# Kernel tuning notes

Hardware: AMD Instinct MI355X
Metric: run time of the kernel (lower is better)

Reference implementation:

```python
import jax, jax.numpy as jnp
import numpy as np

N, K, D = 32768, 8192, 64


def setup_inputs() -> dict:
    key = jax.random.key(0)
    k1, k2, k3 = jax.random.split(key, 3)
    z = jax.random.normal(k1, (N, D), dtype=jnp.float32)
    # Riemannian sensitivity weight per sample (positive scalar from decoder VJP norms)
    g_weight = jax.random.uniform(k2, (N,), dtype=jnp.float32)
    # codebook: nn.Embedding(num_embeddings, embedding_dim), weight ~ N(0,1)
    embedding = jax.random.normal(k3, (K, D), dtype=jnp.float32)
    return {"z": z, "g_weight": g_weight, "embedding": embedding}


def reference(z, g_weight, embedding):
    # d(z, e) = ||z||^2 + ||e||^2 - 2 z e^T  -> [N, K]
    z_flat = z.reshape(-1, embedding.shape[1])
    distances = (
        jnp.sum(z_flat * z_flat, axis=1, keepdims=True)
        + jnp.sum(embedding * embedding, axis=1)
        - 2.0 * jnp.matmul(z_flat, embedding.T)
    )
    # Riemannian scaling: d_R = d * G(z)
    riemannian_distances = distances * g_weight[:, None]
    return jnp.argmin(riemannian_distances, axis=1)
```

## Files before the change

kernel.cpp:

```cpp
#include <hip/hip_runtime.h>
#include <hip/hip_fp16.h>
#include <cfloat>
#include <climits>


typedef short  s16x8  __attribute__((ext_vector_type(8)));
typedef float  f32x16 __attribute__((ext_vector_type(16)));

static constexpr int N_ = 32768;
static constexpr int K_ = 8192;
static constexpr int D_ = 64;
static constexpr int NTILES = K_ / 32;
static constexpr int REC_SLOTS = 576;
static constexpr size_t REC_BYTES = (size_t)NTILES * REC_SLOTS * 16;
static constexpr float FLAG_MARGIN = 0.001953125f;
static constexpr float RESID_SCALE = 1024.0f;
static constexpr float RESID_INV   = 0.0009765625f;

struct alignas(16) Part3 { float b1, b2; int i1, pad; };

__device__ __forceinline__ short f2h_s(float x) {
    __half h = __float2half(x);
    return (short)__half_as_short(h);
}
__device__ __forceinline__ float h2f_s(short s) {
    __half h = __short_as_half((unsigned short)s);
    return __half2float(h);
}

__global__ void rq_prep(const float* __restrict__ emb, s16x8* __restrict__ recs)
{
    __shared__ double sp[32][8];
    const int tile = blockIdx.x;
    const int t = threadIdx.x;
    const int c = t >> 3, q = t & 7;
    const int f = q >> 1, h = q & 1;
    const float* src = emb + (size_t)(tile * 32 + c) * D_ + q * 8;
    float4 a = ((const float4*)src)[0];
    float4 b = ((const float4*)src)[1];
    float e[8] = {a.x, a.y, a.z, a.w, b.x, b.y, b.z, b.w};
    s16x8 u1, u2;
    double s = 0.0;
    #pragma unroll
    for (int j = 0; j < 8; ++j) {
        __half h1 = __float2half(e[j]);
        float r = e[j] - __half2float(h1);
        u1[j] = (short)__half_as_short(h1);
        u2[j] = f2h_s(r * RESID_SCALE);
        s = fma((double)e[j], (double)e[j], s);
    }
    const size_t rb = (size_t)tile * REC_SLOTS;
    recs[rb + f * 64 + h * 32 + c] = u1;
    recs[rb + 320 + f * 64 + h * 32 + c] = u2;
    sp[c][q] = s;
    __syncthreads();
    if (t < 32) {
        double se = 0.0;
        #pragma unroll
        for (int j = 0; j < 8; ++j) se += sp[t][j];
        se *= 0.5;
        float sf = (float)se;
        __half sh = __float2half(sf);
        float  sr = sf - __half2float(sh);
        s16x8 v;
        #pragma unroll
        for (int j = 0; j < 8; ++j) v[j] = 0;
        v[0] = (short)__half_as_short(sh);
        v[1] = f2h_s(sr);
        recs[rb + 256 + t] = v;
    } else if (t < 64) {
        s16x8 v;
        #pragma unroll
        for (int j = 0; j < 8; ++j) v[j] = 0;
        recs[rb + 256 + t] = v;
    }
}

__global__ __launch_bounds__(256)
void rq_main(const float* __restrict__ z,
             const s16x8* __restrict__ recs,
             Part3* __restrict__ parts,
             int tpb )
{
    __shared__ s16x8 lbuf[2][REC_SLOTS];
    const int tid  = threadIdx.x;
    const int wave = tid >> 6, lane = tid & 63;
    const int col  = lane & 31, h = lane >> 5;
    const int slice = blockIdx.y;
    const int tile0 = slice * tpb;
    const int rowbase = blockIdx.x * 128 + wave * 32;
    const int zrow = rowbase + col;

    s16x8 zn1[4], zn2[4];
    #pragma unroll
    for (int f = 0; f < 4; ++f) {
        const float* src = z + (size_t)zrow * D_ + f * 16 + h * 8;
        float4 a = ((const float4*)src)[0];
        float4 b = ((const float4*)src)[1];
        float e[8] = {a.x, a.y, a.z, a.w, b.x, b.y, b.z, b.w};
        #pragma unroll
        for (int j = 0; j < 8; ++j) {
            float zn = -e[j];
            __half h1 = __float2half(zn);
            zn1[f][j] = (short)__half_as_short(h1);
            zn2[f][j] = f2h_s((zn - __half2float(h1)) * RESID_SCALE);
        }
    }
    s16x8 bse;
    #pragma unroll
    for (int j = 0; j < 8; ++j) bse[j] = 0;
    if (h == 0) { bse[0] = (short)0x3C00; bse[1] = (short)0x3C00; }

    {
        const size_t gb = (size_t)tile0 * REC_SLOTS;
        lbuf[0][tid]       = recs[gb + tid];
        lbuf[0][256 + tid] = recs[gb + 256 + tid];
        if (tid < 64) lbuf[0][512 + tid] = recs[gb + 512 + tid];
    }
    __syncthreads();

    float b1 = FLT_MAX, b2 = FLT_MAX;
    int   i1 = INT_MAX;

    for (int t = 0; t < tpb; ++t) {
        const int cb = t & 1, nb = cb ^ 1;
        const bool pf = (t + 1 < tpb);
        s16x8 r0, r1, r2;
        if (pf) {
            const size_t gb = (size_t)(tile0 + t + 1) * REC_SLOTS;
            r0 = recs[gb + tid];
            r1 = recs[gb + 256 + tid];
            if (tid < 64) r2 = recs[gb + 512 + tid];
        }

        s16x8 ea[4], e2a[4], sea;
        #pragma unroll
        for (int f = 0; f < 4; ++f) ea[f]  = lbuf[cb][f * 64 + lane];
        sea = lbuf[cb][256 + lane];
        #pragma unroll
        for (int f = 0; f < 4; ++f) e2a[f] = lbuf[cb][320 + f * 64 + lane];

        f32x16 acc, acc2;
        #pragma unroll
        for (int r = 0; r < 16; ++r) { acc[r] = 0.0f; acc2[r] = 0.0f; }
        #pragma unroll
        for (int f = 0; f < 4; ++f)
            acc = __builtin_amdgcn_mfma_f32_32x32x16_f16(ea[f], zn1[f], acc, 0, 0, 0);
        acc = __builtin_amdgcn_mfma_f32_32x32x16_f16(sea, bse, acc, 0, 0, 0);
        #pragma unroll
        for (int f = 0; f < 4; ++f)
            acc2 = __builtin_amdgcn_mfma_f32_32x32x16_f16(e2a[f], zn1[f], acc2, 0, 0, 0);
        #pragma unroll
        for (int f = 0; f < 4; ++f)
            acc2 = __builtin_amdgcn_mfma_f32_32x32x16_f16(ea[f], zn2[f], acc2, 0, 0, 0);

        const int cbase = (tile0 + t) * 32 + 4 * h;
        #pragma unroll
        for (int r = 0; r < 16; ++r) {
            float v = acc[r] + acc2[r] * RESID_INV;
            int cr = cbase + (r & 3) + 8 * (r >> 2);
            b2 = fminf(b2, fmaxf(v, b1));
            bool lt = v < b1;
            i1 = lt ? cr : i1;
            b1 = fminf(b1, v);
        }

        if (pf) {
            lbuf[nb][tid]       = r0;
            lbuf[nb][256 + tid] = r1;
            if (tid < 64) lbuf[nb][512 + tid] = r2;
        }
        __syncthreads();
    }

    float ob1 = __shfl_xor(b1, 32);
    float ob2 = __shfl_xor(b2, 32);
    int   oi1 = __shfl_xor(i1, 32);
    float nb2 = fminf(fminf(b2, ob2), fmaxf(b1, ob1));
    if (ob1 < b1 || (ob1 == b1 && oi1 < i1)) { b1 = ob1; i1 = oi1; }
    b2 = nb2;
    if (lane < 32) {
        Part3 p; p.b1 = b1; p.b2 = b2; p.i1 = i1; p.pad = 0;
        parts[(size_t)slice * N_ + (rowbase + lane)] = p;
    }
}

__global__ void rq_merge(const Part3* __restrict__ parts,
                         const float* __restrict__ g,
                         int* __restrict__ out,
                         int* __restrict__ counter,
                         int* __restrict__ list,
                         int nsl, int maxf)
{
    int row = blockIdx.x * 256 + threadIdx.x;
    Part3 p = parts[row];
    float b1 = p.b1, b2 = p.b2; int i1 = p.i1;
    for (int s = 1; s < nsl; ++s) {
        Part3 q = parts[(size_t)s * N_ + row];
        float m2 = fminf(fminf(b2, q.b2), fmaxf(b1, q.b1));
        if (q.b1 < b1) { b1 = q.b1; i1 = q.i1; }
        b2 = m2;
    }
    if (g[row] == 0.0f) { out[row] = 0; return; }
    out[row] = i1;
    if (b2 - b1 < FLAG_MARGIN) {
        int idx = atomicAdd(counter, 1);
        if (idx < maxf) list[idx] = row;
    }
}

__global__ __launch_bounds__(256)
void rq_cleanup_part(const float* __restrict__ z,
                     const float* __restrict__ emb,
                     const int* __restrict__ counter,
                     const int* __restrict__ list,
                     double* __restrict__ vparts,
                     int* __restrict__ iparts,
                     int maxf)
{
    int cnt = *counter; if (cnt > maxf) cnt = maxf;
    const int jobs = cnt * 8;
    const int wid  = (blockIdx.x * 256 + threadIdx.x) >> 6;
    const int lane = threadIdx.x & 63;
    const int nw   = gridDim.x * 4;

    for (int j = wid; j < jobs; j += nw) {
        const int row = list[j >> 3];
        const int sl  = j & 7;
        float zr[64];
        {
            const float4* zp = reinterpret_cast<const float4*>(z + (size_t)row * D_);
            #pragma unroll
            for (int q = 0; q < 16; ++q) {
                float4 v = zp[q];
                zr[4*q] = v.x; zr[4*q+1] = v.y; zr[4*q+2] = v.z; zr[4*q+3] = v.w;
            }
        }
        double bv = DBL_MAX; int bi = INT_MAX;
        for (int i = 0; i < 16; ++i) {
            const int c = sl * 1024 + i * 64 + lane;
            const float4* ep = reinterpret_cast<const float4*>(emb + (size_t)c * D_);
            double sd0 = 0, sd1 = 0, sq0 = 0, sq1 = 0;
            #pragma unroll
            for (int q = 0; q < 16; ++q) {
                float4 ev = ep[q];
                sd0 = fma((double)ev.x, (double)zr[4*q+0], sd0);
                sq0 = fma((double)ev.x, (double)ev.x, sq0);
                sd1 = fma((double)ev.y, (double)zr[4*q+1], sd1);
                sq1 = fma((double)ev.y, (double)ev.y, sq1);
                sd0 = fma((double)ev.z, (double)zr[4*q+2], sd0);
                sq0 = fma((double)ev.z, (double)ev.z, sq0);
                sd1 = fma((double)ev.w, (double)zr[4*q+3], sd1);
                sq1 = fma((double)ev.w, (double)ev.w, sq1);
            }
            double v = 0.5 * (sq0 + sq1) - (sd0 + sd1);
            if (v < bv) { bv = v; bi = c; }
        }
        #pragma unroll
        for (int m = 1; m < 64; m <<= 1) {
            double ov = __shfl_xor(bv, m);
            int    oi = __shfl_xor(bi, m);
            if (ov < bv || (ov == bv && oi < bi)) { bv = ov; bi = oi; }
        }
        if (lane == 0) { vparts[j] = bv; iparts[j] = bi; }
    }
}

__global__ void rq_cleanup_fin(const int* __restrict__ counter,
                               const int* __restrict__ list,
                               const double* __restrict__ vparts,
                               const int* __restrict__ iparts,
                               int* __restrict__ out, int maxf)
{
    int cnt = *counter; if (cnt > maxf) cnt = maxf;
    int j = blockIdx.x * 256 + threadIdx.x;
    if (j >= cnt) return;
    double bv = vparts[j * 8]; int bi = iparts[j * 8];
    #pragma unroll
    for (int s = 1; s < 8; ++s) {
        double v = vparts[j * 8 + s]; int i = iparts[j * 8 + s];
        if (v < bv || (v == bv && i < bi)) { bv = v; bi = i; }
    }
    out[list[j]] = bi;
}

__global__ __launch_bounds__(256, 4)
void rq_fallback(const float* __restrict__ z,
                 const float* __restrict__ emb,
                 const float* __restrict__ g,
                 int* __restrict__ out)
{
    __shared__ float  lds_e[64][64];
    __shared__ double lds_se[64];
    const int tid = threadIdx.x;
    const int row = blockIdx.x * 256 + tid;
    float zr[64];
    {
        const float4* zp = reinterpret_cast<const float4*>(z + (size_t)row * D_);
        #pragma unroll
        for (int j = 0; j < 16; ++j) {
            float4 v = zp[j];
            zr[4*j] = v.x; zr[4*j+1] = v.y; zr[4*j+2] = v.z; zr[4*j+3] = v.w;
        }
    }
    float best32 = FLT_MAX; double bestv = DBL_MAX; int bestidx = 0;
    for (int t = 0; t < K_; t += 64) {
        __syncthreads();
        {
            const float4* src = reinterpret_cast<const float4*>(emb + (size_t)t * D_);
            float4* dst = reinterpret_cast<float4*>(&lds_e[0][0]);
            #pragma unroll
            for (int j = 0; j < 4; ++j) dst[tid + j * 256] = src[tid + j * 256];
        }
        if (tid < 64) {
            const float* er = emb + (size_t)(t + tid) * D_;
            double s = 0;
            for (int d = 0; d < 64; ++d) s = fma((double)er[d], (double)er[d], s);
            lds_se[tid] = 0.5 * s;
        }
        __syncthreads();
        float cv0 = FLT_MAX, cv1 = FLT_MAX, cv2 = FLT_MAX;
        int ck0 = 0, ck1 = 0, ck2 = 0;
        for (int kk = 0; kk < 64; ++kk) {
            const float4* ep = reinterpret_cast<const float4*>(&lds_e[kk][0]);
            float a0 = 0, a1 = 0, a2 = 0, a3 = 0;
            #pragma unroll
            for (int j = 0; j < 16; ++j) {
                float4 e4 = ep[j];
                a0 = fmaf(zr[4*j], e4.x, a0);   a1 = fmaf(zr[4*j+1], e4.y, a1);
                a2 = fmaf(zr[4*j+2], e4.z, a2); a3 = fmaf(zr[4*j+3], e4.w, a3);
            }
            float val = (float)lds_se[kk] - ((a0 + a1) + (a2 + a3));
            if (val < best32 + 0.0625f) {
                cv2 = cv1; ck2 = ck1; cv1 = cv0; ck1 = ck0;
                cv0 = val; ck0 = kk;
                best32 = fminf(best32, val);
            }
        }
        const float thr = best32 + 0.0625f;
        #pragma unroll
        for (int r = 0; r < 3; ++r) {
            float cv = (r == 0) ? cv2 : (r == 1) ? cv1 : cv0;
            int   ck = (r == 0) ? ck2 : (r == 1) ? ck1 : ck0;
            if (cv < thr) {
                const float4* ep = reinterpret_cast<const float4*>(&lds_e[ck][0]);
                double s0 = 0, s1 = 0, s2 = 0, s3 = 0;
                #pragma unroll
                for (int j = 0; j < 16; ++j) {
                    float4 e4 = ep[j];
                    s0 = fma((double)zr[4*j],   (double)e4.x, s0);
                    s1 = fma((double)zr[4*j+1], (double)e4.y, s1);
                    s2 = fma((double)zr[4*j+2], (double)e4.z, s2);
                    s3 = fma((double)zr[4*j+3], (double)e4.w, s3);
                }
                double vd = lds_se[ck] - ((s0 + s1) + (s2 + s3));
                int kidx = t + ck;
                if (vd < bestv) { bestv = vd; bestidx = kidx; }
                else if (vd == bestv && kidx < bestidx) bestidx = kidx;
            }
        }
    }
    out[row] = (g[row] == 0.0f) ? 0 : bestidx;
}

extern "C" void kernel_launch(void* const* d_in, const int* in_sizes, int n_in,
                              void* d_out, int out_size, void* d_ws, size_t ws_size,
                              hipStream_t stream)
{
    const float* z   = (const float*)d_in[0];
    const float* g   = (const float*)d_in[1];
    const float* emb = (const float*)d_in[2];
    int* out = (int*)d_out;

    auto need = [&](int s, int mf) {
        return REC_BYTES + (size_t)s * N_ * sizeof(Part3) + 64
             + (size_t)mf * 4 + (size_t)mf * 8 * 8 + (size_t)mf * 8 * 4;
    };
    int nsl = 0, maxf = 0;
    const int nsls[3]  = {4, 2, 1};
    const int maxfs[2] = {16384, 2048};
    for (int a = 0; a < 3 && !nsl; ++a)
        for (int b = 0; b < 2; ++b)
            if (need(nsls[a], maxfs[b]) <= ws_size) { nsl = nsls[a]; maxf = maxfs[b]; break; }

    if (!nsl) {
        rq_fallback<<<N_ / 256, 256, 0, stream>>>(z, emb, g, out);
        return;
    }

    char* w = (char*)d_ws;
    s16x8*  recs    = (s16x8*)w;                              w += REC_BYTES;
    Part3*  parts   = (Part3*)w;                              w += (size_t)nsl * N_ * sizeof(Part3);
    int*    counter = (int*)w;                                w += 64;
    int*    list    = (int*)w;                                w += (size_t)maxf * 4;
    double* vparts  = (double*)w;                             w += (size_t)maxf * 8 * 8;
    int*    iparts  = (int*)w;

    rq_prep<<<NTILES, 256, 0, stream>>>(emb, recs);
    hipMemsetAsync(counter, 0, sizeof(int), stream);
    rq_main<<<dim3(N_ / 128, nsl), 256, 0, stream>>>(z, recs, parts, NTILES / nsl);
    rq_merge<<<N_ / 256, 256, 0, stream>>>(parts, g, out, counter, list, nsl, maxf);
    rq_cleanup_part<<<1024, 256, 0, stream>>>(z, emb, counter, list, vparts, iparts, maxf);
    rq_cleanup_fin<<<128, 256, 0, stream>>>(counter, list, vparts, iparts, out, maxf);
}
```

Before: 165.9 us.

## Interleave MFMA chains, shrink argmin bookkeeping, raise occupancy and slice count

The two MFMA accumulation chains are now interleaved so independent instructions can hide each other's latency, and both start from a shared zero accumulator. The argmin update uses fmed3 and a compact tile/row code that is decoded once after the loop. Launch bounds now request 8 waves per SIMD, up to 8 K-slices are allowed, the counter memset is folded into the prep kernel, and the cleanup grid is halved. Each change targets a different cost (MFMA latency, VALU work in the hot loop, occupancy, an extra launch). More slices add merge traffic, and the occupancy hint may force register spills.

```diff
diff --git a/kernel.cpp b/kernel.cpp
--- a/kernel.cpp
+++ b/kernel.cpp
@@ -23,16 +23,16 @@
     __half h = __float2half(x);
     return (short)__half_as_short(h);
 }
-__device__ __forceinline__ float h2f_s(short s) {
-    __half h = __short_as_half((unsigned short)s);
-    return __half2float(h);
-}
-
-__global__ void rq_prep(const float* __restrict__ emb, s16x8* __restrict__ recs)
+
+#define MFMA16(A, B, C) __builtin_amdgcn_mfma_f32_32x32x16_f16((A), (B), (C), 0, 0, 0)
+
+__global__ void rq_prep(const float* __restrict__ emb, s16x8* __restrict__ recs,
+                        int* __restrict__ counter)
 {
     __shared__ double sp[32][8];
     const int tile = blockIdx.x;
     const int t = threadIdx.x;
+    if (tile == 0 && t == 0) *counter = 0;
     const int c = t >> 3, q = t & 7;
     const int f = q >> 1, h = q & 1;
     const float* src = emb + (size_t)(tile * 32 + c) * D_ + q * 8;
@@ -76,7 +76,7 @@
     }
 }
 
-__global__ __launch_bounds__(256)
+__global__ __launch_bounds__(256, 8)
 void rq_main(const float* __restrict__ z,
              const s16x8* __restrict__ recs,
              Part3* __restrict__ parts,
@@ -110,6 +110,10 @@
     #pragma unroll
     for (int j = 0; j < 8; ++j) bse[j] = 0;
     if (h == 0) { bse[0] = (short)0x3C00; bse[1] = (short)0x3C00; }
+
+    f32x16 zacc;
+    #pragma unroll
+    for (int r = 0; r < 16; ++r) zacc[r] = 0.0f;
 
     {
         const size_t gb = (size_t)tile0 * REC_SLOTS;
@@ -141,27 +145,27 @@
         for (int f = 0; f < 4; ++f) e2a[f] = lbuf[cb][320 + f * 64 + lane];
 
         f32x16 acc, acc2;
-        #pragma unroll
-        for (int r = 0; r < 16; ++r) { acc[r] = 0.0f; acc2[r] = 0.0f; }
-        #pragma unroll
-        for (int f = 0; f < 4; ++f)
-            acc = __builtin_amdgcn_mfma_f32_32x32x16_f16(ea[f], zn1[f], acc, 0, 0, 0);
-        acc = __builtin_amdgcn_mfma_f32_32x32x16_f16(sea, bse, acc, 0, 0, 0);
-        #pragma unroll
-        for (int f = 0; f < 4; ++f)
-            acc2 = __builtin_amdgcn_mfma_f32_32x32x16_f16(e2a[f], zn1[f], acc2, 0, 0, 0);
-        #pragma unroll
-        for (int f = 0; f < 4; ++f)
-            acc2 = __builtin_amdgcn_mfma_f32_32x32x16_f16(ea[f], zn2[f], acc2, 0, 0, 0);
-
-        const int cbase = (tile0 + t) * 32 + 4 * h;
+        acc  = MFMA16(sea,    bse,    zacc);
+        acc2 = MFMA16(e2a[0], zn1[0], zacc);
+        acc  = MFMA16(ea[0],  zn1[0], acc);
+        acc2 = MFMA16(e2a[1], zn1[1], acc2);
+        acc  = MFMA16(ea[1],  zn1[1], acc);
+        acc2 = MFMA16(e2a[2], zn1[2], acc2);
+        acc  = MFMA16(ea[2],  zn1[2], acc);
+        acc2 = MFMA16(e2a[3], zn1[3], acc2);
+        acc  = MFMA16(ea[3],  zn1[3], acc);
+        acc2 = MFMA16(ea[0],  zn2[0], acc2);
+        acc2 = MFMA16(ea[1],  zn2[1], acc2);
+        acc2 = MFMA16(ea[2],  zn2[2], acc2);
+        acc2 = MFMA16(ea[3],  zn2[3], acc2);
+
         #pragma unroll
         for (int r = 0; r < 16; ++r) {
-            float v = acc[r] + acc2[r] * RESID_INV;
-            int cr = cbase + (r & 3) + 8 * (r >> 2);
-            b2 = fminf(b2, fmaxf(v, b1));
+            float v = fmaf(acc2[r], RESID_INV, acc[r]);
+            const int enc = (t << 4) | r;
+            b2 = __builtin_amdgcn_fmed3f(v, b1, b2);
             bool lt = v < b1;
-            i1 = lt ? cr : i1;
+            i1 = lt ? enc : i1;
             b1 = fminf(b1, v);
         }
 
@@ -171,6 +175,11 @@
             if (tid < 64) lbuf[nb][512 + tid] = r2;
         }
         __syncthreads();
+    }
+
+    {
+        const int tt = i1 >> 4, rr = i1 & 15;
+        i1 = (tile0 + tt) * 32 + 4 * h + (rr & 3) + 8 * (rr >> 2);
     }
 
     float ob1 = __shfl_xor(b1, 32);
@@ -377,9 +386,9 @@
              + (size_t)mf * 4 + (size_t)mf * 8 * 8 + (size_t)mf * 8 * 4;
     };
     int nsl = 0, maxf = 0;
-    const int nsls[3]  = {4, 2, 1};
+    const int nsls[4]  = {8, 4, 2, 1};
     const int maxfs[2] = {16384, 2048};
-    for (int a = 0; a < 3 && !nsl; ++a)
+    for (int a = 0; a < 4 && !nsl; ++a)
         for (int b = 0; b < 2; ++b)
             if (need(nsls[a], maxfs[b]) <= ws_size) { nsl = nsls[a]; maxf = maxfs[b]; break; }
 
@@ -396,10 +405,9 @@
     double* vparts  = (double*)w;                             w += (size_t)maxf * 8 * 8;
     int*    iparts  = (int*)w;
 
-    rq_prep<<<NTILES, 256, 0, stream>>>(emb, recs);
-    hipMemsetAsync(counter, 0, sizeof(int), stream);
+    rq_prep<<<NTILES, 256, 0, stream>>>(emb, recs, counter);
     rq_main<<<dim3(N_ / 128, nsl), 256, 0, stream>>>(z, recs, parts, NTILES / nsl);
     rq_merge<<<N_ / 256, 256, 0, stream>>>(parts, g, out, counter, list, nsl, maxf);
-    rq_cleanup_part<<<1024, 256, 0, stream>>>(z, emb, counter, list, vparts, iparts, maxf);
+    rq_cleanup_part<<<512, 256, 0, stream>>>(z, emb, counter, list, vparts, iparts, maxf);
     rq_cleanup_fin<<<128, 256, 0, stream>>>(counter, list, vparts, iparts, out, maxf);
 }
```

Result: slower. 387.3 us (+133.5%).
